# Kernel optimization log

Hardware: AMD Instinct MI355X
Metric: run time of the kernel (lower is better)

The kernel has to match this reference:

```python
import jax, jax.numpy as jnp
import numpy as np

N, E, B = 100000, 400000, 1024
NF, EF, H, C, D = 32, 16, 256, 256, 6
LN_EPS = 1e-5


def setup_inputs() -> dict:
    key = jax.random.key(0)
    ks = jax.random.split(key, 32)
    def nrm(k, shape, s=0.05):
        return jax.random.normal(k, shape, jnp.float32) * s
    inp = {}
    inp['node_x'] = jax.random.normal(ks[0], (N, NF), jnp.float32)
    inp['edge_e'] = jax.random.normal(ks[1], (E, EF), jnp.float32)
    inp['t'] = jax.random.uniform(ks[2], (B,), jnp.float32)
    inp['n_index'] = jnp.sort(jax.random.randint(ks[3], (N,), 0, B))
    inp['src'] = jax.random.randint(ks[4], (E,), 0, N)
    inp['dst'] = jax.random.randint(ks[5], (E,), 0, N)
    inp['in_conv_w'] = nrm(ks[6], (NF, H), 0.1)
    inp['in_conv_b'] = jnp.zeros((H,), jnp.float32)
    inp['edge_w'] = nrm(ks[7], (EF, H), 0.1)
    inp['edge_b'] = jnp.zeros((H,), jnp.float32)
    inp['t_w1'] = nrm(ks[8], (128, C))
    inp['t_b1'] = jnp.zeros((C,), jnp.float32)
    inp['t_w2'] = nrm(ks[9], (C, C))
    inp['t_b2'] = jnp.zeros((C,), jnp.float32)
    inp['conv1_w'] = nrm(ks[10], (D, H, H))
    inp['conv1_b'] = jnp.zeros((D, H), jnp.float32)
    inp['conv2_w'] = nrm(ks[11], (D, H, H))
    inp['conv2_b'] = jnp.zeros((D, H), jnp.float32)
    inp['ln1_g'] = jnp.ones((D, H), jnp.float32)
    inp['ln1_b'] = jnp.zeros((D, H), jnp.float32)
    inp['ln2_g'] = jnp.ones((D, H), jnp.float32)
    inp['ln2_b'] = jnp.zeros((D, H), jnp.float32)
    inp['film1_w'] = nrm(ks[12], (D, C, 2 * H))
    inp['film1_b'] = nrm(ks[13], (D, 2 * H), 0.01)
    inp['film2_w'] = nrm(ks[14], (D, C, 2 * H))
    inp['film2_b'] = nrm(ks[15], (D, 2 * H), 0.01)
    # NOTE: source zero-inits the head; we use small random weights so the
    # baseline output is non-degenerate (init detail, not forward math).
    inp['head_w'] = nrm(ks[16], (H, 1))
    inp['head_b'] = jnp.zeros((1,), jnp.float32)
    return inp


def reference(node_x, edge_e, t, n_index, src, dst,
              in_conv_w, in_conv_b, edge_w, edge_b,
              t_w1, t_b1, t_w2, t_b2,
              conv1_w, conv1_b, conv2_w, conv2_b,
              ln1_g, ln1_b, ln2_g, ln2_b,
              film1_w, film1_b, film2_w, film2_b,
              head_w, head_b):
    n = node_x.shape[0]
    b = t.shape[0]
    ones_e = jnp.ones(src.shape[0], node_x.dtype)
    # DGL GraphConv norm='both': D_dst^{-1/2} A (D_src^{-1/2} X) W + b, degrees clamped to >=1
    deg_out = jnp.clip(jax.ops.segment_sum(ones_e, src, num_segments=n), 1.0)
    deg_in = jnp.clip(jax.ops.segment_sum(ones_e, dst, num_segments=n), 1.0)
    no = deg_out ** -0.5
    ni = deg_in ** -0.5

    def gconv(x, W, bia):
        agg = jax.ops.segment_sum((x * no[:, None])[src], dst, num_segments=n)
        return (agg * ni[:, None]) @ W + bia

    def lnorm(x, g, bia):
        mu = jnp.mean(x, -1, keepdims=True)
        v = jnp.mean(jnp.square(x - mu), -1, keepdims=True)
        return (x - mu) * jax.lax.rsqrt(v + LN_EPS) * g + bia

    def film(x, cond, fw, fb):
        gb = cond @ fw + fb           # (B, 2H)
        gam, bet = jnp.split(gb, 2, axis=-1)
        return x * (1.0 + gam[n_index]) + bet[n_index]

    # sinusoidal time embedding + MLP
    half = t_w1.shape[0] // 2
    freqs = jnp.exp(-jnp.log(1000.0) * jnp.arange(half, dtype=jnp.float32) / half)
    a = (t * 1000.0)[:, None] * freqs[None, :]
    emb = jnp.concatenate([jnp.sin(a), jnp.cos(a)], axis=-1)   # (B, 128)
    cond = jax.nn.silu(emb @ t_w1 + t_b1) @ t_w2 + t_b2        # (B, C)

    h = gconv(node_x, in_conv_w, in_conv_b)                    # (N, H)
    e_h = edge_e @ edge_w + edge_b                             # (E, H)
    e_mean = jax.ops.segment_sum(e_h, dst, num_segments=n) / deg_in[:, None]
    h = h + e_mean

    for i in range(conv1_w.shape[0]):
        # NOTE: source module has a bug: conv2 consumes the block INPUT (not the
        # conv1 branch), so the conv1/norm1/film1/silu result is dead. Replicated
        # faithfully; jit DCEs the dead branch.
        _dead = jax.nn.silu(film(lnorm(gconv(h, conv1_w[i], conv1_b[i]), ln1_g[i], ln1_b[i]), cond, film1_w[i], film1_b[i]))
        h2 = jax.nn.silu(film(lnorm(gconv(h, conv2_w[i], conv2_b[i]), ln2_g[i], ln2_b[i]), cond, film2_w[i], film2_b[i]))
        h = h2 + h  # skip = Identity since in_dim == out_dim

    ones_n = jnp.ones(n, h.dtype)
    cnt = jnp.clip(jax.ops.segment_sum(ones_n, n_index, num_segments=b), 1.0)
    g_mean = jax.ops.segment_sum(h, n_index, num_segments=b) / cnt[:, None]
    return g_mean @ head_w + head_b  # scale = 1.0
```

## Files before the change

### kernel.cpp

```cpp
#include <hip/hip_runtime.h>
#include <math.h>

#define HDIM 256
#define NLAYERS 6

typedef __attribute__((ext_vector_type(8))) short short8v;
typedef __attribute__((ext_vector_type(16))) float f32x16;

__device__ __forceinline__ float silu_(float x){ return x * (1.f/(1.f+__expf(-x))); }

__device__ __forceinline__ unsigned short f2bf(float f){
  unsigned u = __float_as_uint(f);
  u += 0x7FFF + ((u>>16)&1);
  return (unsigned short)(u>>16);
}
__device__ __forceinline__ float bf2f(unsigned short b){ return __uint_as_float(((unsigned)b)<<16); }

__device__ __forceinline__ void gload_lds16(const void* g, void* l){
  __builtin_amdgcn_global_load_lds((const __attribute__((address_space(1))) void*)g,
                                   (__attribute__((address_space(3))) void*)l, 16, 0, 0);
}

__global__ void k_count(const int* __restrict__ src, const int* __restrict__ dst, int E,
                        int* __restrict__ cnt_out, int* __restrict__ cnt_in){
  int e = blockIdx.x*256 + threadIdx.x;
  if(e < E){
    atomicAdd(&cnt_out[src[e]], 1);
    atomicAdd(&cnt_in[dst[e]], 1);
  }
}

__global__ __launch_bounds__(256) void k_scan1(const int* __restrict__ cnt_in,
                                               int* __restrict__ partial, int N){
  __shared__ int s[256];
  int b = blockIdx.x, tid = threadIdx.x;
  int i0 = b*1024 + tid*4;
  int sum = 0;
  #pragma unroll
  for(int j=0;j<4;j++){ int i=i0+j; if(i<N) sum += cnt_in[i]; }
  s[tid] = sum; __syncthreads();
  for(int off=128; off; off>>=1){ if(tid<off) s[tid]+=s[tid+off]; __syncthreads(); }
  if(tid==0) partial[b] = s[0];
}
__global__ __launch_bounds__(256) void k_scan2(int* __restrict__ partial,
                                               int* __restrict__ csr_off, int nb, int N){
  __shared__ int s[256];
  int tid = threadIdx.x;
  int v = (tid<nb) ? partial[tid] : 0;
  s[tid] = v; __syncthreads();
  for(int off=1; off<256; off<<=1){
    int t = (tid>=off) ? s[tid-off] : 0;
    __syncthreads(); s[tid] += t; __syncthreads();
  }
  if(tid<nb) partial[tid] = s[tid] - v;
  if(tid==255) csr_off[N] = s[255];
}
__global__ __launch_bounds__(256) void k_scan3(const int* __restrict__ cnt_in,
                                               const int* __restrict__ partial,
                                               int* __restrict__ csr_off, int N){
  __shared__ int s[256];
  int b = blockIdx.x, tid = threadIdx.x;
  int i0 = b*1024 + tid*4;
  int c[4];
  #pragma unroll
  for(int j=0;j<4;j++){ int i=i0+j; c[j] = (i<N) ? cnt_in[i] : 0; }
  int tot = c[0]+c[1]+c[2]+c[3];
  s[tid] = tot; __syncthreads();
  for(int off=1; off<256; off<<=1){
    int t = (tid>=off) ? s[tid-off] : 0;
    __syncthreads(); s[tid] += t; __syncthreads();
  }
  int run = s[tid] - tot + partial[b];
  #pragma unroll
  for(int j=0;j<4;j++){
    int i = i0+j;
    if(i<N) csr_off[i] = run;
    run += c[j];
  }
}

__global__ void k_prep(const int* __restrict__ cnt_out, const int* __restrict__ cnt_in,
                       const int* __restrict__ csr_off, const int* __restrict__ n_index,
                       float* __restrict__ no, float* __restrict__ ni,
                       int* __restrict__ csr_pos, int* __restrict__ gcnt, int N){
  int v = blockIdx.x*256 + threadIdx.x;
  if(v < N){
    no[v] = rsqrtf((float)max(cnt_out[v],1));
    ni[v] = rsqrtf((float)max(cnt_in[v],1));
    csr_pos[v] = csr_off[v];
    atomicAdd(&gcnt[n_index[v]], 1);
  }
}

__global__ void k_fill(const int* __restrict__ src, const int* __restrict__ dst, int E,
                       int* __restrict__ csr_pos, int* __restrict__ csr_src,
                       int* __restrict__ csr_eid){
  int e = blockIdx.x*256 + threadIdx.x;
  if(e < E){
    int p = atomicAdd(&csr_pos[dst[e]], 1);
    csr_src[p] = src[e];
    csr_eid[p] = e;
  }
}

__global__ __launch_bounds__(256) void k_cond(const float* __restrict__ t,
        const float* __restrict__ w1, const float* __restrict__ b1,
        const float* __restrict__ w2, const float* __restrict__ b2,
        float* __restrict__ cond){
  __shared__ float emb[128];
  __shared__ float hid[256];
  int b = blockIdx.x, tid = threadIdx.x;
  float tv = t[b] * 1000.f;
  if(tid < 128){
    int k = tid & 63;
    float fr = expf(-logf(1000.f) * (float)k * (1.f/64.f));
    float a = tv * fr;
    emb[tid] = (tid < 64) ? sinf(a) : cosf(a);
  }
  __syncthreads();
  {
    float s = b1[tid];
    for(int k=0;k<128;k++) s += emb[k] * w1[k*HDIM + tid];
    hid[tid] = silu_(s);
  }
  __syncthreads();
  {
    float s = b2[tid];
    for(int k=0;k<256;k++) s += hid[k] * w2[k*HDIM + tid];
    cond[(size_t)b*HDIM + tid] = s;
  }
}

template<int K>
__global__ __launch_bounds__(256) void k_gemm_f32(
    const float* __restrict__ A, int lda,
    const float* __restrict__ W, int ldw,
    const float* __restrict__ bias,
    float* __restrict__ out, int ldo, int M, int mode,
    unsigned short* __restrict__ out_bf){
  if(mode == 1){
    int c = blockIdx.y;
    W    += (size_t)(c>>1)*131072 + (size_t)(c&1)*256;
    bias += (size_t)(c>>1)*512 + (size_t)(c&1)*256;
    out  += (size_t)c*1024*256;
  }
  __shared__ float As[64][36];
  __shared__ float Ws[32][256];
  const int tid = threadIdx.x;
  const int rg = tid >> 4;
  const int cg = tid & 15;
  const int row0 = blockIdx.x * 64;

  float4 acc[4][4];
  #pragma unroll
  for(int i=0;i<4;i++)
    #pragma unroll
    for(int m=0;m<4;m++) acc[i][m] = make_float4(0.f,0.f,0.f,0.f);

  const int ar = tid >> 2;
  const int ac = (tid & 3) * 8;
  const int wr = tid >> 3;
  const int wc = (tid & 7) * 32;

  for(int kk=0; kk<K; kk+=32){
    {
      int gr = row0 + ar;
      float4 v0 = make_float4(0.f,0.f,0.f,0.f), v1 = v0;
      if(gr < M){
        v0 = *(const float4*)&A[(size_t)gr*lda + kk + ac];
        v1 = *(const float4*)&A[(size_t)gr*lda + kk + ac + 4];
      }
      *(float4*)&As[ar][ac]   = v0;
      *(float4*)&As[ar][ac+4] = v1;
    }
    #pragma unroll
    for(int u=0;u<8;u++)
      *(float4*)&Ws[wr][wc + u*4] = *(const float4*)&W[(size_t)(kk+wr)*ldw + wc + u*4];
    __syncthreads();
    #pragma unroll 8
    for(int k=0;k<32;k++){
      float a0 = As[rg*4+0][k];
      float a1 = As[rg*4+1][k];
      float a2 = As[rg*4+2][k];
      float a3 = As[rg*4+3][k];
      #pragma unroll
      for(int m=0;m<4;m++){
        float4 w = *(const float4*)&Ws[k][cg*4 + m*64];
        acc[0][m].x += a0*w.x; acc[0][m].y += a0*w.y; acc[0][m].z += a0*w.z; acc[0][m].w += a0*w.w;
        acc[1][m].x += a1*w.x; acc[1][m].y += a1*w.y; acc[1][m].z += a1*w.z; acc[1][m].w += a1*w.w;
        acc[2][m].x += a2*w.x; acc[2][m].y += a2*w.y; acc[2][m].z += a2*w.z; acc[2][m].w += a2*w.w;
        acc[3][m].x += a3*w.x; acc[3][m].y += a3*w.y; acc[3][m].z += a3*w.z; acc[3][m].w += a3*w.w;
      }
    }
    __syncthreads();
  }

  const int c0 = cg * 4;
  #pragma unroll
  for(int i=0;i<4;i++){
    const int gr = row0 + rg*4 + i;
    if(gr >= M) continue;
    #pragma unroll
    for(int m=0;m<4;m++){
      const int c = c0 + m*64;
      float4 b4 = *(const float4*)&bias[c];
      float4 o = make_float4(acc[i][m].x+b4.x, acc[i][m].y+b4.y,
                             acc[i][m].z+b4.z, acc[i][m].w+b4.w);
      if(out) *(float4*)&out[(size_t)gr*ldo + c] = o;
      if(out_bf)
        *(ushort4*)&out_bf[(size_t)gr*ldo + c] =
            make_ushort4(f2bf(o.x), f2bf(o.y), f2bf(o.z), f2bf(o.w));
    }
  }
}

__global__ void k_wcat(const float* __restrict__ in_w, const float* __restrict__ ew,
                       const float* __restrict__ eb, float* __restrict__ wcat){
  int idx = blockIdx.x*256 + threadIdx.x;
  int r = idx>>8, c = idx&255;
  float v = 0.f;
  if(r < 32) v = in_w[r*HDIM + c];
  else if(r < 48) v = ew[(r-32)*HDIM + c];
  else if(r == 48) v = eb[c];
  wcat[idx] = v;
}

__global__ void k_w2b(const float* __restrict__ W, unsigned short* __restrict__ hi_,
                      unsigned short* __restrict__ lo_){
  int idx = blockIdx.x*256 + threadIdx.x;
  int i = idx >> 16, r = idx & 65535;
  int n = r >> 8, k = r & 255;
  float v = W[((size_t)i*256 + k)*256 + n];
  unsigned short h = f2bf(v);
  float lo = v - bf2f(h);
  hi_[((size_t)i*256 + n)*256 + k] = h;
  lo_[((size_t)i*256 + n)*256 + k] = f2bf(lo);
}

__global__ __launch_bounds__(256) void k_init_agg(const float* __restrict__ node_x,
    const float* __restrict__ edge_e,
    const int* __restrict__ csr_off, const int* __restrict__ csr_src, const int* __restrict__ csr_eid,
    const float* __restrict__ no, const float* __restrict__ ni, const int* __restrict__ cnt_in,
    float* __restrict__ A48, int N){
  int v = blockIdx.x*4 + (threadIdx.x>>6);
  if(v >= N) return;
  int lane = threadIdx.x & 63;
  int beg = csr_off[v], end = csr_off[v+1];
  float acc = 0.f;
  for(int p=beg; p<end; p++){
    int s = csr_src[p]; int e = csr_eid[p];
    if(lane < 32)      acc += node_x[(size_t)s*32 + lane] * no[s];
    else if(lane < 48) acc += edge_e[(size_t)e*16 + (lane-32)];
  }
  int ci = cnt_in[v];
  float out;
  if(lane < 32)      out = acc * ni[v];
  else if(lane < 48) out = acc * (1.f/(float)max(ci,1));
  else if(lane == 48) out = (ci>0) ? 1.f : 0.f;
  else out = 0.f;
  A48[(size_t)v*64 + lane] = out;
}

__global__ __launch_bounds__(256) void k_gather_bf(const unsigned short* __restrict__ hbf,
   const int* __restrict__ csr_off, const int* __restrict__ csr_src,
   const float* __restrict__ no, const float* __restrict__ ni,
   unsigned short* __restrict__ ahi, int N, int Npad){
  int v = blockIdx.x*4 + (threadIdx.x>>6);
  if(v >= Npad) return;
  int lane = threadIdx.x & 63;
  float4 acc = make_float4(0.f,0.f,0.f,0.f);
  if(v < N){
    int beg = csr_off[v], end = csr_off[v+1];
    for(int p=beg; p<end; p++){
      int s = csr_src[p];
      float w = no[s];
      ushort4 x = *(const ushort4*)&hbf[(size_t)s*HDIM + lane*4];
      acc.x += bf2f(x.x)*w; acc.y += bf2f(x.y)*w;
      acc.z += bf2f(x.z)*w; acc.w += bf2f(x.w)*w;
    }
    float sc = ni[v];
    acc.x*=sc; acc.y*=sc; acc.z*=sc; acc.w*=sc;
  }
  ushort4 hv = make_ushort4(f2bf(acc.x), f2bf(acc.y), f2bf(acc.z), f2bf(acc.w));
  *(ushort4*)&ahi[(size_t)v*HDIM + lane*4] = hv;
}

template<bool LAST>
__global__ __launch_bounds__(256) void k_layer_mfma(
    const unsigned short* __restrict__ Ahi,
    const unsigned short* __restrict__ Bhi, const unsigned short* __restrict__ Blo,
    const float* __restrict__ bias, const float* __restrict__ lng, const float* __restrict__ lnb,
    const float* __restrict__ gamL, const float* __restrict__ betL,
    const int* __restrict__ n_index, unsigned short* __restrict__ hbf,
    const float* __restrict__ hw, float* __restrict__ gsum, int N){
  __shared__ __align__(16) char smem[40960];
  float* zbuf = (float*)smem;
  const int tid = threadIdx.x;
  const int w = tid >> 6, l = tid & 63;
  const int half = l >> 5, lcol = l & 31;
  const int row0 = blockIdx.x * 64;
  const int colb = w * 64;

  const size_t bb = (size_t)(colb + lcol)*HDIM + half*8;

  short8v Bh0[4], Bh1[4], Bl0[4], Bl1[4];
  #define LOADB(t, s) { \
    Bh0[s] = *(const short8v*)&Bhi[bb + (t)*16]; \
    Bh1[s] = *(const short8v*)&Bhi[bb + 32*HDIM + (t)*16]; \
    Bl0[s] = *(const short8v*)&Blo[bb + (t)*16]; \
    Bl1[s] = *(const short8v*)&Blo[bb + 32*HDIM + (t)*16]; }
  LOADB(0,0) LOADB(1,1) LOADB(2,2)

  {
    const int m = tid & 31;
    const int rofs = tid >> 5;
    #pragma unroll
    for(int chunk=0; chunk<8; chunk++){
      const int row = chunk*8 + rofs;
      const int msw = (m & 24) | ((m ^ row) & 7);
      const size_t src = (size_t)(row0 + row)*HDIM + msw*8;
      gload_lds16(&Ahi[src], (char*)smem + chunk*4096 + tid*16);
    }
  }
  __syncthreads();

  f32x16 acc[2][2] = {};
  const char* baseH = (const char*)smem;

  #pragma unroll
  for(int t=0; t<16; t++){
    if(t < 13) LOADB(t+3, (t+3)&3)
    const int s = t & 3;
    const int g = t*2 + half;
    const int slot = (g & 24) | ((g ^ lcol) & 7);
    short8v ah0 = *(const short8v*)(baseH + lcol*512 + slot*16);
    short8v ah1 = *(const short8v*)(baseH + (32+lcol)*512 + slot*16);

    acc[0][0] = __builtin_amdgcn_mfma_f32_32x32x16_bf16(ah0, Bh0[s], acc[0][0], 0,0,0);
    acc[0][1] = __builtin_amdgcn_mfma_f32_32x32x16_bf16(ah0, Bh1[s], acc[0][1], 0,0,0);
    acc[1][0] = __builtin_amdgcn_mfma_f32_32x32x16_bf16(ah1, Bh0[s], acc[1][0], 0,0,0);
    acc[1][1] = __builtin_amdgcn_mfma_f32_32x32x16_bf16(ah1, Bh1[s], acc[1][1], 0,0,0);
    acc[0][0] = __builtin_amdgcn_mfma_f32_32x32x16_bf16(ah0, Bl0[s], acc[0][0], 0,0,0);
    acc[0][1] = __builtin_amdgcn_mfma_f32_32x32x16_bf16(ah0, Bl1[s], acc[0][1], 0,0,0);
    acc[1][0] = __builtin_amdgcn_mfma_f32_32x32x16_bf16(ah1, Bl0[s], acc[1][0], 0,0,0);
    acc[1][1] = __builtin_amdgcn_mfma_f32_32x32x16_bf16(ah1, Bl1[s], acc[1][1], 0,0,0);
  }
  #undef LOADB

  float bias_c[2];
  bias_c[0] = bias[colb + lcol];
  bias_c[1] = bias[colb + 32 + lcol];

  const int qr = l >> 4, lc = l & 15;
  float4 lngc[4], lnbc[4], hwc[4];
  #pragma unroll
  for(int j=0;j<4;j++){
    lngc[j] = *(const float4*)&lng[lc*4 + j*64];
    lnbc[j] = *(const float4*)&lnb[lc*4 + j*64];
    if(LAST) hwc[j] = *(const float4*)&hw[lc*4 + j*64];
  }

  #pragma unroll
  for(int pass=0; pass<2; pass++){
    __syncthreads();
    #pragma unroll
    for(int r=0; r<16; r++){
      const int rl = (r&3) + 8*(r>>2) + 4*half;
      zbuf[rl*HDIM + colb      + lcol] = acc[pass][0][r] + bias_c[0];
      zbuf[rl*HDIM + colb + 32 + lcol] = acc[pass][1][r] + bias_c[1];
    }
    __syncthreads();
    #pragma unroll
    for(int it=0; it<2; it++){
      const int row = w*8 + it*4 + qr;
      const int grow = row0 + pass*32 + row;
      const bool ok = grow < N;
      const int bidx = ok ? n_index[grow] : 0;
      float4 z[4];
      #pragma unroll
      for(int j=0;j<4;j++) z[j] = *(const float4*)&zbuf[row*HDIM + lc*4 + j*64];
      float s = 0.f, q = 0.f;
      #pragma unroll
      for(int j=0;j<4;j++){
        s += z[j].x + z[j].y + z[j].z + z[j].w;
        q += z[j].x*z[j].x + z[j].y*z[j].y + z[j].z*z[j].z + z[j].w*z[j].w;
      }
      #pragma unroll
      for(int off=1; off<16; off<<=1){ s += __shfl_xor(s, off, 16); q += __shfl_xor(q, off, 16); }
      const float mu = s * (1.f/256.f);
      const float rs = rsqrtf(fmaxf(q*(1.f/256.f) - mu*mu, 0.f) + 1e-5f);
      float4 g4[4], b4[4];
      #pragma unroll
      for(int j=0;j<4;j++){
        g4[j] = *(const float4*)&gamL[(size_t)bidx*HDIM + lc*4 + j*64];
        b4[j] = *(const float4*)&betL[(size_t)bidx*HDIM + lc*4 + j*64];
      }
      float4 o[4];
      #pragma unroll
      for(int j=0;j<4;j++){
        float zn;
        zn = (z[j].x-mu)*rs*lngc[j].x + lnbc[j].x; o[j].x = silu_(zn*(1.f+g4[j].x)+b4[j].x);
        zn = (z[j].y-mu)*rs*lngc[j].y + lnbc[j].y; o[j].y = silu_(zn*(1.f+g4[j].y)+b4[j].y);
        zn = (z[j].z-mu)*rs*lngc[j].z + lnbc[j].z; o[j].z = silu_(zn*(1.f+g4[j].z)+b4[j].z);
        zn = (z[j].w-mu)*rs*lngc[j].w + lnbc[j].w; o[j].w = silu_(zn*(1.f+g4[j].w)+b4[j].w);
      }
      if(LAST){
        float rd = 0.f;
        #pragma unroll
        for(int j=0;j<4;j++){
          ushort4 hv = ok ? *(const ushort4*)&hbf[(size_t)grow*HDIM + lc*4 + j*64]
                          : make_ushort4(0,0,0,0);
          rd += (o[j].x+bf2f(hv.x))*hwc[j].x + (o[j].y+bf2f(hv.y))*hwc[j].y
              + (o[j].z+bf2f(hv.z))*hwc[j].z + (o[j].w+bf2f(hv.w))*hwc[j].w;
        }
        #pragma unroll
        for(int off=1; off<16; off<<=1) rd += __shfl_xor(rd, off, 16);
        if(lc == 0 && ok) atomicAdd(&gsum[bidx], rd);
      } else {
        if(ok){
          #pragma unroll
          for(int j=0;j<4;j++){
            ushort4 hv = *(const ushort4*)&hbf[(size_t)grow*HDIM + lc*4 + j*64];
            float ox = o[j].x + bf2f(hv.x), oy = o[j].y + bf2f(hv.y);
            float oz = o[j].z + bf2f(hv.z), ow = o[j].w + bf2f(hv.w);
            *(ushort4*)&hbf[(size_t)grow*HDIM + lc*4 + j*64] =
                make_ushort4(f2bf(ox), f2bf(oy), f2bf(oz), f2bf(ow));
          }
        }
      }
    }
  }
}

__global__ void k_final(const float* __restrict__ gsum, const int* __restrict__ gcnt,
                        const float* __restrict__ hb, float* __restrict__ out, int B){
  int b = blockIdx.x*256 + threadIdx.x;
  if(b < B) out[b] = gsum[b] / (float)max(gcnt[b],1) + hb[0];
}

extern "C" void kernel_launch(void* const* d_in, const int* in_sizes, int n_in,
                              void* d_out, int out_size, void* d_ws, size_t ws_size,
                              hipStream_t stream){
  const float* node_x   = (const float*)d_in[0];
  const float* edge_e   = (const float*)d_in[1];
  const float* t        = (const float*)d_in[2];
  const int*   n_index  = (const int*)d_in[3];
  const int*   src      = (const int*)d_in[4];
  const int*   dst      = (const int*)d_in[5];
  const float* in_conv_w= (const float*)d_in[6];
  const float* in_conv_b= (const float*)d_in[7];
  const float* edge_w   = (const float*)d_in[8];
  const float* edge_b   = (const float*)d_in[9];
  const float* t_w1     = (const float*)d_in[10];
  const float* t_b1     = (const float*)d_in[11];
  const float* t_w2     = (const float*)d_in[12];
  const float* t_b2     = (const float*)d_in[13];
  const float* conv2_w  = (const float*)d_in[16];
  const float* conv2_b  = (const float*)d_in[17];
  const float* ln2_g    = (const float*)d_in[20];
  const float* ln2_b    = (const float*)d_in[21];
  const float* film2_w  = (const float*)d_in[24];
  const float* film2_b  = (const float*)d_in[25];
  const float* head_w   = (const float*)d_in[26];
  const float* head_b   = (const float*)d_in[27];

  const int N = in_sizes[3];
  const int E = in_sizes[4];
  const int B = in_sizes[2];
  const int Npad = (N + 63) & ~63;

  char* w = (char*)d_ws;
  auto alloc = [&](size_t bytes)->char*{
    char* p = w; w += (bytes + 255) & ~(size_t)255; return p;
  };
  int*   cnt_out = (int*)  alloc((size_t)N*4);
  int*   cnt_in  = (int*)  alloc((size_t)N*4);
  float* no      = (float*)alloc((size_t)N*4);
  float* ni      = (float*)alloc((size_t)N*4);
  int*   csr_off = (int*)  alloc((size_t)(N+1)*4);
  int*   csr_pos = (int*)  alloc((size_t)N*4);
  int*   csr_src = (int*)  alloc((size_t)E*4);
  int*   csr_eid = (int*)  alloc((size_t)E*4);
  int*   partial = (int*)  alloc((size_t)256*4);
  float* cond    = (float*)alloc((size_t)B*HDIM*4);
  float* gbX     = (float*)alloc((size_t)12*B*HDIM*4);
  float* gsum    = (float*)alloc((size_t)B*4);
  int*   gcnt    = (int*)  alloc((size_t)B*4);
  unsigned short* hbf    = (unsigned short*)alloc((size_t)Npad*HDIM*2);
  unsigned short* agg_hi = (unsigned short*)alloc((size_t)Npad*HDIM*2);
  unsigned short* Wthi   = (unsigned short*)alloc((size_t)NLAYERS*HDIM*HDIM*2);
  unsigned short* Wtlo   = (unsigned short*)alloc((size_t)NLAYERS*HDIM*HDIM*2);
  float* wcat    = (float*)alloc((size_t)64*HDIM*4);
  float* A48     = (float*)alloc((size_t)Npad*64*4);

  hipMemsetAsync(cnt_out, 0, (size_t)N*4, stream);
  hipMemsetAsync(cnt_in,  0, (size_t)N*4, stream);
  hipMemsetAsync(gsum,    0, (size_t)B*4, stream);
  hipMemsetAsync(gcnt,    0, (size_t)B*4, stream);

  int gE = (E+255)/256, gN = (N+255)/256;
  int nb1 = (N+1023)/1024;
  k_count<<<gE,256,0,stream>>>(src, dst, E, cnt_out, cnt_in);
  k_scan1<<<nb1,256,0,stream>>>(cnt_in, partial, N);
  k_scan2<<<1,256,0,stream>>>(partial, csr_off, nb1, N);
  k_scan3<<<nb1,256,0,stream>>>(cnt_in, partial, csr_off, N);
  k_prep<<<gN,256,0,stream>>>(cnt_out, cnt_in, csr_off, n_index, no, ni, csr_pos, gcnt, N);
  k_fill<<<gE,256,0,stream>>>(src, dst, E, csr_pos, csr_src, csr_eid);

  k_cond<<<B,256,0,stream>>>(t, t_w1, t_b1, t_w2, t_b2, cond);
  k_gemm_f32<256><<<dim3(B/64,12),256,0,stream>>>(cond, HDIM, film2_w, 512, film2_b,
                                                  gbX, HDIM, B, 1, nullptr);

  k_w2b<<<NLAYERS*HDIM*HDIM/256,256,0,stream>>>(conv2_w, Wthi, Wtlo);
  k_wcat<<<64,256,0,stream>>>(in_conv_w, edge_w, edge_b, wcat);
  k_init_agg<<<(N+3)/4,256,0,stream>>>(node_x, edge_e, csr_off, csr_src, csr_eid,
                                       no, ni, cnt_in, A48, N);
  k_gemm_f32<64><<<Npad/64,256,0,stream>>>(A48, 64, wcat, HDIM, in_conv_b,
                                           nullptr, HDIM, N, 0, hbf);

  for(int i=0;i<NLAYERS;i++){
    k_gather_bf<<<Npad/4,256,0,stream>>>(hbf, csr_off, csr_src, no, ni, agg_hi, N, Npad);
    if(i < NLAYERS-1)
      k_layer_mfma<false><<<Npad/64,256,0,stream>>>(agg_hi,
          Wthi + (size_t)i*HDIM*HDIM, Wtlo + (size_t)i*HDIM*HDIM,
          conv2_b + (size_t)i*HDIM,
          ln2_g + (size_t)i*HDIM, ln2_b + (size_t)i*HDIM,
          gbX + (size_t)(2*i)*B*HDIM, gbX + (size_t)(2*i+1)*B*HDIM,
          n_index, hbf, head_w, gsum, N);
    else
      k_layer_mfma<true><<<Npad/64,256,0,stream>>>(agg_hi,
          Wthi + (size_t)i*HDIM*HDIM, Wtlo + (size_t)i*HDIM*HDIM,
          conv2_b + (size_t)i*HDIM,
          ln2_g + (size_t)i*HDIM, ln2_b + (size_t)i*HDIM,
          gbX + (size_t)(2*i)*B*HDIM, gbX + (size_t)(2*i+1)*B*HDIM,
          n_index, hbf, head_w, gsum, N);
  }

  k_final<<<(B+255)/256,256,0,stream>>>(gsum, gcnt, head_b, (float*)d_out, B);
}
```

Baseline: 1.297 ms.

## Fuse neighbor gather into layer MFMA kernel with ping-pong feature buffers

Removes the separate gather kernel and performs the CSR neighbor aggregation directly inside the per-layer MFMA kernel. Each wave aggregates 16 rows, two rows interleaved at a time for more memory-level parallelism, and writes the bf16 results straight into the swizzled LDS tile. This avoids writing and re-reading the aggregated tensor through global memory and saves one launch per layer. Because other blocks now read node features while this layer runs, the output goes to a second buffer and the two buffers alternate between layers. The cost is a serialized, latency-bound gather phase ahead of the GEMM in each block, with lower parallelism than the old one-node-per-wave gather.

```diff
diff --git a/kernel.cpp b/kernel.cpp
--- a/kernel.cpp
+++ b/kernel.cpp
@@ -15,11 +15,6 @@
   return (unsigned short)(u>>16);
 }
 __device__ __forceinline__ float bf2f(unsigned short b){ return __uint_as_float(((unsigned)b)<<16); }
-
-__device__ __forceinline__ void gload_lds16(const void* g, void* l){
-  __builtin_amdgcn_global_load_lds((const __attribute__((address_space(1))) void*)g,
-                                   (__attribute__((address_space(3))) void*)l, 16, 0, 0);
-}
 
 __global__ void k_count(const int* __restrict__ src, const int* __restrict__ dst, int E,
                         int* __restrict__ cnt_out, int* __restrict__ cnt_in){
@@ -261,37 +256,15 @@
   A48[(size_t)v*64 + lane] = out;
 }
 
-__global__ __launch_bounds__(256) void k_gather_bf(const unsigned short* __restrict__ hbf,
-   const int* __restrict__ csr_off, const int* __restrict__ csr_src,
-   const float* __restrict__ no, const float* __restrict__ ni,
-   unsigned short* __restrict__ ahi, int N, int Npad){
-  int v = blockIdx.x*4 + (threadIdx.x>>6);
-  if(v >= Npad) return;
-  int lane = threadIdx.x & 63;
-  float4 acc = make_float4(0.f,0.f,0.f,0.f);
-  if(v < N){
-    int beg = csr_off[v], end = csr_off[v+1];
-    for(int p=beg; p<end; p++){
-      int s = csr_src[p];
-      float w = no[s];
-      ushort4 x = *(const ushort4*)&hbf[(size_t)s*HDIM + lane*4];
-      acc.x += bf2f(x.x)*w; acc.y += bf2f(x.y)*w;
-      acc.z += bf2f(x.z)*w; acc.w += bf2f(x.w)*w;
-    }
-    float sc = ni[v];
-    acc.x*=sc; acc.y*=sc; acc.z*=sc; acc.w*=sc;
-  }
-  ushort4 hv = make_ushort4(f2bf(acc.x), f2bf(acc.y), f2bf(acc.z), f2bf(acc.w));
-  *(ushort4*)&ahi[(size_t)v*HDIM + lane*4] = hv;
-}
-
 template<bool LAST>
-__global__ __launch_bounds__(256) void k_layer_mfma(
-    const unsigned short* __restrict__ Ahi,
+__global__ __launch_bounds__(256) void k_layer_fused(
+    const int* __restrict__ csr_off, const int* __restrict__ csr_src,
+    const float* __restrict__ no, const float* __restrict__ ni,
+    const unsigned short* __restrict__ Hin, unsigned short* __restrict__ Hout,
     const unsigned short* __restrict__ Bhi, const unsigned short* __restrict__ Blo,
     const float* __restrict__ bias, const float* __restrict__ lng, const float* __restrict__ lnb,
     const float* __restrict__ gamL, const float* __restrict__ betL,
-    const int* __restrict__ n_index, unsigned short* __restrict__ hbf,
+    const int* __restrict__ n_index,
     const float* __restrict__ hw, float* __restrict__ gsum, int N){
   __shared__ __align__(16) char smem[40960];
   float* zbuf = (float*)smem;
@@ -312,14 +285,36 @@
   LOADB(0,0) LOADB(1,1) LOADB(2,2)
 
   {
-    const int m = tid & 31;
-    const int rofs = tid >> 5;
+    const int gw = l >> 1;
     #pragma unroll
-    for(int chunk=0; chunk<8; chunk++){
-      const int row = chunk*8 + rofs;
-      const int msw = (m & 24) | ((m ^ row) & 7);
-      const size_t src = (size_t)(row0 + row)*HDIM + msw*8;
-      gload_lds16(&Ahi[src], (char*)smem + chunk*4096 + tid*16);
+    for(int rr=0; rr<16; rr+=2){
+      const int r0 = w*16 + rr, r1 = r0 + 1;
+      const int v0 = row0 + r0, v1 = row0 + r1;
+      float4 a0 = make_float4(0.f,0.f,0.f,0.f), a1 = a0;
+      int p0 = (v0<N)?csr_off[v0]:0, e0 = (v0<N)?csr_off[v0+1]:0;
+      int p1 = (v1<N)?csr_off[v1]:0, e1 = (v1<N)?csr_off[v1+1]:0;
+      for(;;){
+        bool b0 = p0<e0, b1 = p1<e1;
+        if(!(b0|b1)) break;
+        int s0=0, s1=0;
+        if(b0) s0 = csr_src[p0];
+        if(b1) s1 = csr_src[p1];
+        ushort4 x0, x1;
+        if(b0) x0 = *(const ushort4*)&Hin[(size_t)s0*HDIM + l*4];
+        if(b1) x1 = *(const ushort4*)&Hin[(size_t)s1*HDIM + l*4];
+        if(b0){ float wg=no[s0];
+          a0.x+=bf2f(x0.x)*wg; a0.y+=bf2f(x0.y)*wg; a0.z+=bf2f(x0.z)*wg; a0.w+=bf2f(x0.w)*wg; p0++; }
+        if(b1){ float wg=no[s1];
+          a1.x+=bf2f(x1.x)*wg; a1.y+=bf2f(x1.y)*wg; a1.z+=bf2f(x1.z)*wg; a1.w+=bf2f(x1.w)*wg; p1++; }
+      }
+      if(v0<N){ float sc=ni[v0]; a0.x*=sc; a0.y*=sc; a0.z*=sc; a0.w*=sc; }
+      if(v1<N){ float sc=ni[v1]; a1.x*=sc; a1.y*=sc; a1.z*=sc; a1.w*=sc; }
+      const int s0l = (gw & 24) | ((gw ^ r0) & 7);
+      const int s1l = (gw & 24) | ((gw ^ r1) & 7);
+      *(ushort4*)(smem + r0*512 + s0l*16 + (l&1)*8) =
+          make_ushort4(f2bf(a0.x), f2bf(a0.y), f2bf(a0.z), f2bf(a0.w));
+      *(ushort4*)(smem + r1*512 + s1l*16 + (l&1)*8) =
+          make_ushort4(f2bf(a1.x), f2bf(a1.y), f2bf(a1.z), f2bf(a1.w));
     }
   }
   __syncthreads();
@@ -408,7 +403,7 @@
         float rd = 0.f;
         #pragma unroll
         for(int j=0;j<4;j++){
-          ushort4 hv = ok ? *(const ushort4*)&hbf[(size_t)grow*HDIM + lc*4 + j*64]
+          ushort4 hv = ok ? *(const ushort4*)&Hin[(size_t)grow*HDIM + lc*4 + j*64]
                           : make_ushort4(0,0,0,0);
           rd += (o[j].x+bf2f(hv.x))*hwc[j].x + (o[j].y+bf2f(hv.y))*hwc[j].y
               + (o[j].z+bf2f(hv.z))*hwc[j].z + (o[j].w+bf2f(hv.w))*hwc[j].w;
@@ -420,10 +415,10 @@
         if(ok){
           #pragma unroll
           for(int j=0;j<4;j++){
-            ushort4 hv = *(const ushort4*)&hbf[(size_t)grow*HDIM + lc*4 + j*64];
+            ushort4 hv = *(const ushort4*)&Hin[(size_t)grow*HDIM + lc*4 + j*64];
             float ox = o[j].x + bf2f(hv.x), oy = o[j].y + bf2f(hv.y);
             float oz = o[j].z + bf2f(hv.z), ow = o[j].w + bf2f(hv.w);
-            *(ushort4*)&hbf[(size_t)grow*HDIM + lc*4 + j*64] =
+            *(ushort4*)&Hout[(size_t)grow*HDIM + lc*4 + j*64] =
                 make_ushort4(f2bf(ox), f2bf(oy), f2bf(oz), f2bf(ow));
           }
         }
@@ -486,8 +481,8 @@
   float* gbX     = (float*)alloc((size_t)12*B*HDIM*4);
   float* gsum    = (float*)alloc((size_t)B*4);
   int*   gcnt    = (int*)  alloc((size_t)B*4);
-  unsigned short* hbf    = (unsigned short*)alloc((size_t)Npad*HDIM*2);
-  unsigned short* agg_hi = (unsigned short*)alloc((size_t)Npad*HDIM*2);
+  unsigned short* hbfA   = (unsigned short*)alloc((size_t)Npad*HDIM*2);
+  unsigned short* hbfB   = (unsigned short*)alloc((size_t)Npad*HDIM*2);
   unsigned short* Wthi   = (unsigned short*)alloc((size_t)NLAYERS*HDIM*HDIM*2);
   unsigned short* Wtlo   = (unsigned short*)alloc((size_t)NLAYERS*HDIM*HDIM*2);
   float* wcat    = (float*)alloc((size_t)64*HDIM*4);
@@ -516,24 +511,27 @@
   k_init_agg<<<(N+3)/4,256,0,stream>>>(node_x, edge_e, csr_off, csr_src, csr_eid,
                                        no, ni, cnt_in, A48, N);
   k_gemm_f32<64><<<Npad/64,256,0,stream>>>(A48, 64, wcat, HDIM, in_conv_b,
-                                           nullptr, HDIM, N, 0, hbf);
+                                           nullptr, HDIM, N, 0, hbfA);
 
   for(int i=0;i<NLAYERS;i++){
-    k_gather_bf<<<Npad/4,256,0,stream>>>(hbf, csr_off, csr_src, no, ni, agg_hi, N, Npad);
+    const unsigned short* Hin = (i & 1) ? hbfB : hbfA;
+    unsigned short* Hout      = (i & 1) ? hbfA : hbfB;
     if(i < NLAYERS-1)
-      k_layer_mfma<false><<<Npad/64,256,0,stream>>>(agg_hi,
+      k_layer_fused<false><<<Npad/64,256,0,stream>>>(csr_off, csr_src, no, ni,
+          Hin, Hout,
           Wthi + (size_t)i*HDIM*HDIM, Wtlo + (size_t)i*HDIM*HDIM,
           conv2_b + (size_t)i*HDIM,
           ln2_g + (size_t)i*HDIM, ln2_b + (size_t)i*HDIM,
           gbX + (size_t)(2*i)*B*HDIM, gbX + (size_t)(2*i+1)*B*HDIM,
-          n_index, hbf, head_w, gsum, N);
+          n_index, head_w, gsum, N);
     else
-      k_layer_mfma<true><<<Npad/64,256,0,stream>>>(agg_hi,
+      k_layer_fused<true><<<Npad/64,256,0,stream>>>(csr_off, csr_src, no, ni,
+          Hin, Hout,
           Wthi + (size_t)i*HDIM*HDIM, Wtlo + (size_t)i*HDIM*HDIM,
           conv2_b + (size_t)i*HDIM,
           ln2_g + (size_t)i*HDIM, ln2_b + (size_t)i*HDIM,
           gbX + (size_t)(2*i)*B*HDIM, gbX + (size_t)(2*i+1)*B*HDIM,
-          n_index, hbf, head_w, gsum, N);
+          n_index, head_w, gsum, N);
   }
 
   k_final<<<(B+255)/256,256,0,stream>>>(gsum, gcnt, head_b, (float*)d_out, B);
```

Result: slower. 2.255 ms (+73.8%).

## Halve layer GEMM row tile to 32 and raise occupancy via launch bounds

Applied to the files above, without the earlier changes.

Each layer block now handles 32 rows instead of 64, so it keeps two accumulators instead of four, uses a shallower B prefetch ring (2 stages instead of 4) and a smaller LDS footprint. The launch bounds request 6 waves-per-EU-level occupancy, and LN/head parameters are loaded inside the epilogue loop instead of being held in registers. The aim is more resident blocks to hide memory latency. The cost is that each block reloads the full weight matrix for half as many rows, doubling B traffic per row, and the shallower prefetch exposes more load latency.

```diff
diff --git a/kernel.cpp b/kernel.cpp
--- a/kernel.cpp
+++ b/kernel.cpp
@@ -286,36 +286,35 @@
 }
 
 template<bool LAST>
-__global__ __launch_bounds__(256) void k_layer_mfma(
+__global__ __launch_bounds__(256, 6) void k_layer_mfma(
     const unsigned short* __restrict__ Ahi,
     const unsigned short* __restrict__ Bhi, const unsigned short* __restrict__ Blo,
     const float* __restrict__ bias, const float* __restrict__ lng, const float* __restrict__ lnb,
     const float* __restrict__ gamL, const float* __restrict__ betL,
     const int* __restrict__ n_index, unsigned short* __restrict__ hbf,
     const float* __restrict__ hw, float* __restrict__ gsum, int N){
-  __shared__ __align__(16) char smem[40960];
+  __shared__ __align__(16) char smem[24576];
   float* zbuf = (float*)smem;
   const int tid = threadIdx.x;
   const int w = tid >> 6, l = tid & 63;
   const int half = l >> 5, lcol = l & 31;
-  const int row0 = blockIdx.x * 64;
+  const int row0 = blockIdx.x * 32;
   const int colb = w * 64;
-
   const size_t bb = (size_t)(colb + lcol)*HDIM + half*8;
 
-  short8v Bh0[4], Bh1[4], Bl0[4], Bl1[4];
+  short8v Bh0[2], Bh1[2], Bl0[2], Bl1[2];
   #define LOADB(t, s) { \
     Bh0[s] = *(const short8v*)&Bhi[bb + (t)*16]; \
     Bh1[s] = *(const short8v*)&Bhi[bb + 32*HDIM + (t)*16]; \
     Bl0[s] = *(const short8v*)&Blo[bb + (t)*16]; \
     Bl1[s] = *(const short8v*)&Blo[bb + 32*HDIM + (t)*16]; }
-  LOADB(0,0) LOADB(1,1) LOADB(2,2)
+  LOADB(0,0) LOADB(1,1)
 
   {
     const int m = tid & 31;
     const int rofs = tid >> 5;
     #pragma unroll
-    for(int chunk=0; chunk<8; chunk++){
+    for(int chunk=0; chunk<4; chunk++){
       const int row = chunk*8 + rofs;
       const int msw = (m & 24) | ((m ^ row) & 7);
       const size_t src = (size_t)(row0 + row)*HDIM + msw*8;
@@ -324,56 +323,42 @@
   }
   __syncthreads();
 
-  f32x16 acc[2][2] = {};
+  f32x16 acc0 = {}, acc1 = {};
   const char* baseH = (const char*)smem;
 
   #pragma unroll
   for(int t=0; t<16; t++){
-    if(t < 13) LOADB(t+3, (t+3)&3)
-    const int s = t & 3;
+    if(t < 15) LOADB(t+1, (t+1)&1)
+    const int s = t & 1;
     const int g = t*2 + half;
     const int slot = (g & 24) | ((g ^ lcol) & 7);
     short8v ah0 = *(const short8v*)(baseH + lcol*512 + slot*16);
-    short8v ah1 = *(const short8v*)(baseH + (32+lcol)*512 + slot*16);
-
-    acc[0][0] = __builtin_amdgcn_mfma_f32_32x32x16_bf16(ah0, Bh0[s], acc[0][0], 0,0,0);
-    acc[0][1] = __builtin_amdgcn_mfma_f32_32x32x16_bf16(ah0, Bh1[s], acc[0][1], 0,0,0);
-    acc[1][0] = __builtin_amdgcn_mfma_f32_32x32x16_bf16(ah1, Bh0[s], acc[1][0], 0,0,0);
-    acc[1][1] = __builtin_amdgcn_mfma_f32_32x32x16_bf16(ah1, Bh1[s], acc[1][1], 0,0,0);
-    acc[0][0] = __builtin_amdgcn_mfma_f32_32x32x16_bf16(ah0, Bl0[s], acc[0][0], 0,0,0);
-    acc[0][1] = __builtin_amdgcn_mfma_f32_32x32x16_bf16(ah0, Bl1[s], acc[0][1], 0,0,0);
-    acc[1][0] = __builtin_amdgcn_mfma_f32_32x32x16_bf16(ah1, Bl0[s], acc[1][0], 0,0,0);
-    acc[1][1] = __builtin_amdgcn_mfma_f32_32x32x16_bf16(ah1, Bl1[s], acc[1][1], 0,0,0);
+    acc0 = __builtin_amdgcn_mfma_f32_32x32x16_bf16(ah0, Bh0[s], acc0, 0,0,0);
+    acc1 = __builtin_amdgcn_mfma_f32_32x32x16_bf16(ah0, Bh1[s], acc1, 0,0,0);
+    acc0 = __builtin_amdgcn_mfma_f32_32x32x16_bf16(ah0, Bl0[s], acc0, 0,0,0);
+    acc1 = __builtin_amdgcn_mfma_f32_32x32x16_bf16(ah0, Bl1[s], acc1, 0,0,0);
   }
   #undef LOADB
 
   float bias_c[2];
   bias_c[0] = bias[colb + lcol];
   bias_c[1] = bias[colb + 32 + lcol];
-
   const int qr = l >> 4, lc = l & 15;
-  float4 lngc[4], lnbc[4], hwc[4];
-  #pragma unroll
-  for(int j=0;j<4;j++){
-    lngc[j] = *(const float4*)&lng[lc*4 + j*64];
-    lnbc[j] = *(const float4*)&lnb[lc*4 + j*64];
-    if(LAST) hwc[j] = *(const float4*)&hw[lc*4 + j*64];
-  }
 
   #pragma unroll
   for(int pass=0; pass<2; pass++){
     __syncthreads();
     #pragma unroll
-    for(int r=0; r<16; r++){
-      const int rl = (r&3) + 8*(r>>2) + 4*half;
-      zbuf[rl*HDIM + colb      + lcol] = acc[pass][0][r] + bias_c[0];
-      zbuf[rl*HDIM + colb + 32 + lcol] = acc[pass][1][r] + bias_c[1];
+    for(int r=0; r<8; r++){
+      const int rr = pass*8 + r;
+      const int rl = (rr&3) + 8*((rr>>2)&1) + 4*half;
+      zbuf[rl*HDIM + colb      + lcol] = acc0[rr] + bias_c[0];
+      zbuf[rl*HDIM + colb + 32 + lcol] = acc1[rr] + bias_c[1];
     }
     __syncthreads();
-    #pragma unroll
-    for(int it=0; it<2; it++){
-      const int row = w*8 + it*4 + qr;
-      const int grow = row0 + pass*32 + row;
+    {
+      const int row = w*4 + qr;
+      const int grow = row0 + pass*16 + row;
       const bool ok = grow < N;
       const int bidx = ok ? n_index[grow] : 0;
       float4 z[4];
@@ -389,44 +374,40 @@
       for(int off=1; off<16; off<<=1){ s += __shfl_xor(s, off, 16); q += __shfl_xor(q, off, 16); }
       const float mu = s * (1.f/256.f);
       const float rs = rsqrtf(fmaxf(q*(1.f/256.f) - mu*mu, 0.f) + 1e-5f);
-      float4 g4[4], b4[4];
+      float rd = 0.f;
       #pragma unroll
       for(int j=0;j<4;j++){
-        g4[j] = *(const float4*)&gamL[(size_t)bidx*HDIM + lc*4 + j*64];
-        b4[j] = *(const float4*)&betL[(size_t)bidx*HDIM + lc*4 + j*64];
-      }
-      float4 o[4];
-      #pragma unroll
-      for(int j=0;j<4;j++){
+        const int c = lc*4 + j*64;
+        const float4 lg = *(const float4*)&lng[c];
+        const float4 lb = *(const float4*)&lnb[c];
+        const float4 g4 = *(const float4*)&gamL[(size_t)bidx*HDIM + c];
+        const float4 b4 = *(const float4*)&betL[(size_t)bidx*HDIM + c];
+        float4 o;
         float zn;
-        zn = (z[j].x-mu)*rs*lngc[j].x + lnbc[j].x; o[j].x = silu_(zn*(1.f+g4[j].x)+b4[j].x);
-        zn = (z[j].y-mu)*rs*lngc[j].y + lnbc[j].y; o[j].y = silu_(zn*(1.f+g4[j].y)+b4[j].y);
-        zn = (z[j].z-mu)*rs*lngc[j].z + lnbc[j].z; o[j].z = silu_(zn*(1.f+g4[j].z)+b4[j].z);
-        zn = (z[j].w-mu)*rs*lngc[j].w + lnbc[j].w; o[j].w = silu_(zn*(1.f+g4[j].w)+b4[j].w);
+        zn = (z[j].x-mu)*rs*lg.x + lb.x; o.x = silu_(zn*(1.f+g4.x)+b4.x);
+        zn = (z[j].y-mu)*rs*lg.y + lb.y; o.y = silu_(zn*(1.f+g4.y)+b4.y);
+        zn = (z[j].z-mu)*rs*lg.z + lb.z; o.z = silu_(zn*(1.f+g4.z)+b4.z);
+        zn = (z[j].w-mu)*rs*lg.w + lb.w; o.w = silu_(zn*(1.f+g4.w)+b4.w);
+        if(LAST){
+          ushort4 hv = ok ? *(const ushort4*)&hbf[(size_t)grow*HDIM + c]
+                          : make_ushort4(0,0,0,0);
+          const float4 w4 = *(const float4*)&hw[c];
+          rd += (o.x+bf2f(hv.x))*w4.x + (o.y+bf2f(hv.y))*w4.y
+              + (o.z+bf2f(hv.z))*w4.z + (o.w+bf2f(hv.w))*w4.w;
+        } else {
+          if(ok){
+            ushort4 hv = *(const ushort4*)&hbf[(size_t)grow*HDIM + c];
+            float ox = o.x + bf2f(hv.x), oy = o.y + bf2f(hv.y);
+            float oz = o.z + bf2f(hv.z), ow = o.w + bf2f(hv.w);
+            *(ushort4*)&hbf[(size_t)grow*HDIM + c] =
+                make_ushort4(f2bf(ox), f2bf(oy), f2bf(oz), f2bf(ow));
+          }
+        }
       }
       if(LAST){
-        float rd = 0.f;
-        #pragma unroll
-        for(int j=0;j<4;j++){
-          ushort4 hv = ok ? *(const ushort4*)&hbf[(size_t)grow*HDIM + lc*4 + j*64]
-                          : make_ushort4(0,0,0,0);
-          rd += (o[j].x+bf2f(hv.x))*hwc[j].x + (o[j].y+bf2f(hv.y))*hwc[j].y
-              + (o[j].z+bf2f(hv.z))*hwc[j].z + (o[j].w+bf2f(hv.w))*hwc[j].w;
-        }
         #pragma unroll
         for(int off=1; off<16; off<<=1) rd += __shfl_xor(rd, off, 16);
         if(lc == 0 && ok) atomicAdd(&gsum[bidx], rd);
-      } else {
-        if(ok){
-          #pragma unroll
-          for(int j=0;j<4;j++){
-            ushort4 hv = *(const ushort4*)&hbf[(size_t)grow*HDIM + lc*4 + j*64];
-            float ox = o[j].x + bf2f(hv.x), oy = o[j].y + bf2f(hv.y);
-            float oz = o[j].z + bf2f(hv.z), ow = o[j].w + bf2f(hv.w);
-            *(ushort4*)&hbf[(size_t)grow*HDIM + lc*4 + j*64] =
-                make_ushort4(f2bf(ox), f2bf(oy), f2bf(oz), f2bf(ow));
-          }
-        }
       }
     }
   }
@@ -521,14 +502,14 @@
   for(int i=0;i<NLAYERS;i++){
     k_gather_bf<<<Npad/4,256,0,stream>>>(hbf, csr_off, csr_src, no, ni, agg_hi, N, Npad);
     if(i < NLAYERS-1)
-      k_layer_mfma<false><<<Npad/64,256,0,stream>>>(agg_hi,
+      k_layer_mfma<false><<<Npad/32,256,0,stream>>>(agg_hi,
           Wthi + (size_t)i*HDIM*HDIM, Wtlo + (size_t)i*HDIM*HDIM,
           conv2_b + (size_t)i*HDIM,
           ln2_g + (size_t)i*HDIM, ln2_b + (size_t)i*HDIM,
           gbX + (size_t)(2*i)*B*HDIM, gbX + (size_t)(2*i+1)*B*HDIM,
           n_index, hbf, head_w, gsum, N);
     else
-      k_layer_mfma<true><<<Npad/64,256,0,stream>>>(agg_hi,
+      k_layer_mfma<true><<<Npad/32,256,0,stream>>>(agg_hi,
           Wthi + (size_t)i*HDIM*HDIM, Wtlo + (size_t)i*HDIM*HDIM,
           conv2_b + (size_t)i*HDIM,
           ln2_g + (size_t)i*HDIM, ln2_b + (size_t)i*HDIM,
```

New measurement: 1.728 ms. +33.2%, slower.
